# Performance work log

Hardware: AMD Instinct MI355X
Metric: run time of the kernel (lower is better)

The kernel has to match this reference:

```python
import jax, jax.numpy as jnp
import numpy as np

K = 4            # kNN neighbors (edge_conv k=4)
HEADS = 4
HID = 32
NEG_SLOPE = 0.2  # PyG GATConv leaky_relu default


def knn_idx(x, k):
    # x: [N, C]. Pairwise squared distances via gram trick, self excluded.
    N = x.shape[0]
    sq = jnp.sum(x * x, axis=1)
    d = sq[:, None] + sq[None, :] - 2.0 * (x @ x.T)          # [N, N]
    r = jnp.arange(N)
    d = d.at[r, r].set(jnp.inf)                               # no self in kNN
    _, idx = jax.lax.top_k(-d, k)                             # [N, k] nearest
    return idx


def gat_layer(x, neigh, W, a_src, a_dst, b):
    # x: [N, C]; neigh: [N, k+1] (incl. self loop). PyG GATConv, concat=True.
    N = x.shape[0]
    h = (x @ W).reshape(N, HEADS, HID)                        # [N, H, D]
    asrc = jnp.einsum('nhd,hd->nh', h, a_src)                 # [N, H]
    adst = jnp.einsum('nhd,hd->nh', h, a_dst)                 # [N, H]
    e = jax.nn.leaky_relu(adst[:, None, :] + asrc[neigh], NEG_SLOPE)  # [N, k+1, H]
    attn = jax.nn.softmax(e, axis=1)                          # segment softmax (fixed fan-in)
    out = jnp.einsum('nkh,nkhd->nhd', attn, h[neigh])         # [N, H, D]
    return out.reshape(N, HEADS * HID) + b


def setup_inputs() -> dict:
    key = jax.random.key(0)
    ks = jax.random.split(key, 12)
    B, E, C = 256, 64, 32
    s = 0.1
    return {
        'x': jax.random.normal(ks[0], (B, E, C), jnp.float32),
        # DynamicEdgeConv MLP: Linear(2C->HID), ReLU, Linear(HID->HID)
        'mlp_w1': jax.random.normal(ks[1], (2 * C, HID), jnp.float32) * s,
        'mlp_b1': jnp.zeros((HID,), jnp.float32),
        'mlp_w2': jax.random.normal(ks[2], (HID, HID), jnp.float32) * s,
        'mlp_b2': jnp.zeros((HID,), jnp.float32),
        # GATConv(HID, HID, heads=HEADS, concat=True)
        'gat_w': jax.random.normal(ks[3], (C, HEADS * HID), jnp.float32) * s,
        'gat_asrc': jax.random.normal(ks[4], (HEADS, HID), jnp.float32) * s,
        'gat_adst': jax.random.normal(ks[5], (HEADS, HID), jnp.float32) * s,
        'gat_b': jnp.zeros((HEADS * HID,), jnp.float32),
        # fc: Linear(HID*HEADS -> num_classes)
        'fc_w': jax.random.normal(ks[6], (HEADS * HID, 2), jnp.float32) * s,
        'fc_b': jnp.zeros((2,), jnp.float32),
    }


def reference(x, mlp_w1, mlp_b1, mlp_w2, mlp_b2, gat_w, gat_asrc, gat_adst, gat_b, fc_w, fc_b):
    B, E, C = x.shape
    N = B * E
    xf = x.reshape(N, C)
    idx = knn_idx(xf, K)                                      # [N, K] int32
    # EdgeConv message MLP + max pool (edge_attr is discarded by the original forward)
    xi = xf[:, None, :]                                       # [N, 1, C]
    xj = xf[idx]                                              # [N, K, C]
    ef = jnp.concatenate([jnp.broadcast_to(xi, xj.shape), xj - xi], axis=-1)
    ef = jax.nn.relu(ef @ mlp_w1 + mlp_b1) @ mlp_w2 + mlp_b2
    _edge_attr = ef.max(axis=1)                               # [N, HID], unused downstream
    # GAT with self loops (PyG add_self_loops=True)
    neigh = jnp.concatenate([idx, jnp.arange(N)[:, None]], axis=1)  # [N, K+1]
    h = gat_layer(xf, neigh, gat_w, gat_asrc, gat_adst, gat_b)
    h = jax.nn.elu(h)
    h = h.reshape(B, E, HEADS * HID).mean(axis=1)             # [B, H*D]
    return h @ fc_w + fc_b                                    # [B, num_classes]
```

## Files before the change

### kernel.cpp

```cpp
#include <hip/hip_runtime.h>
#include <math.h>

#define N_PTS   16384
#define NT      1024
#define NCHUNK  32
#define JT_CH   (NT/NCHUNK)
#define SUBT    8
#define NSUB    (JT_CH/SUBT)
#define NS      16

typedef __attribute__((ext_vector_type(4))) float f32x4;
typedef __attribute__((ext_vector_type(8))) _Float16 half8;

union H8 { half8 h; float4 f; };

#define MED3(a,b,c) __builtin_amdgcn_fmed3f((a),(b),(c))

#define INS4(c, A0, A1, A2, A3) {        \
  float n0_ = fmaxf(A0, c);              \
  float n1_ = MED3(A0, A1, c);           \
  float n2_ = MED3(A1, A2, c);           \
  float n3_ = MED3(A2, A3, c);           \
  A0 = n0_; A1 = n1_; A2 = n2_; A3 = n3_; }

__device__ __forceinline__ unsigned long long pack_key(float a, int j) {
  unsigned u = __float_as_uint(a);
  unsigned ord = u ^ (unsigned)(((int)u >> 31) | 0x80000000);
  unsigned m = ~ord;
  return ((unsigned long long)m << 32) | (unsigned)j;
}

__global__ __launch_bounds__(256) void k_prep(
    const float* __restrict__ x, float4* __restrict__ fragHi,
    float4* __restrict__ fragLo, float* __restrict__ nsq,
    unsigned* __restrict__ gcnt, unsigned long long* __restrict__ gbuf,
    unsigned* __restrict__ bcnt)
{
  int p = blockIdx.x * 256 + threadIdx.x;
  const float4* xp = (const float4*)(x + (size_t)p * 32);
  int tile = p >> 4, lb = p & 15;
  float sq = 0.f;
  #pragma unroll
  for (int g = 0; g < 4; ++g) {
    float4 va = xp[g * 2], vb = xp[g * 2 + 1];
    float f[8] = {va.x, va.y, va.z, va.w, vb.x, vb.y, vb.z, vb.w};
    H8 hh, hl;
    #pragma unroll
    for (int e = 0; e < 8; ++e) {
      sq = fmaf(f[e], f[e], sq);
      _Float16 hi = (_Float16)f[e];
      _Float16 lo = (_Float16)(f[e] - (float)hi);
      hh.h[e] = hi; hl.h[e] = hl.h[e] = lo;
    }
    int a = tile * 64 + g * 16 + lb;
    fragHi[a] = hh.f; fragLo[a] = hl.f;
  }
  nsq[p] = -0.5f * sq;
  gcnt[p] = 0u;
  #pragma unroll
  for (int e = 0; e < NS; ++e) gbuf[(size_t)p * NS + e] = ~0ull;
  if (blockIdx.x == 0 && threadIdx.x < NCHUNK) bcnt[threadIdx.x] = 0u;
}

__global__ __launch_bounds__(256, 4) void k_knnA(
    const float4* __restrict__ fragHi, const float4* __restrict__ fragLo,
    const float* __restrict__ nsq, float* __restrict__ cvals)
{
  __shared__ half8 sHi[SUBT * 64];
  __shared__ half8 sLo[SUBT * 64];
  __shared__ float sNq[SUBT * 16];

  const int tid = threadIdx.x;
  const int w = tid >> 6, lane = tid & 63;
  const int grp = lane >> 4, col = lane & 15;
  const int cy = blockIdx.y;
  const int itbase = blockIdx.x * 16 + w * 4;
  const bool blkdiag = ((int)(blockIdx.x >> 1) == cy);

  const half8* fH8 = (const half8*)fragHi;
  const half8* fL8 = (const half8*)fragLo;

  half8 bh[4], bl[4];
  #pragma unroll
  for (int s = 0; s < 4; ++s) {
    bh[s] = fH8[(size_t)(itbase + s) * 64 + lane];
    bl[s] = fL8[(size_t)(itbase + s) * 64 + lane];
  }
  const bool dg0 = (col == grp * 4 + 0), dg1 = (col == grp * 4 + 1);
  const bool dg2 = (col == grp * 4 + 2), dg3 = (col == grp * 4 + 3);

  float La1[4];
  #pragma unroll
  for (int s = 0; s < 4; ++s) La1[s] = -3.4e38f;

  for (int sc = 0; sc < NSUB; ++sc) {
    int jt0 = cy * JT_CH + sc * SUBT;
    __syncthreads();
    const float4* gH = fragHi + (size_t)jt0 * 64;
    const float4* gL = fragLo + (size_t)jt0 * 64;
    float4* dH = (float4*)sHi;
    float4* dL = (float4*)sLo;
    #pragma unroll
    for (int r = 0; r < 2; ++r) {
      dH[tid + r * 256] = gH[tid + r * 256];
      dL[tid + r * 256] = gL[tid + r * 256];
    }
    if (tid < SUBT * 16) sNq[tid] = nsq[jt0 * 16 + tid];
    __syncthreads();

    for (int t = 0; t < SUBT; ++t) {
      half8 ah = sHi[t * 64 + lane];
      half8 al = sLo[t * 64 + lane];
      f32x4 q = *(const f32x4*)&sNq[t * 16 + grp * 4];
      int jt = jt0 + t;
      #pragma unroll
      for (int s = 0; s < 4; ++s) {
        f32x4 acc = __builtin_amdgcn_mfma_f32_16x16x32_f16(ah, bh[s], q, 0, 0, 0);
        acc = __builtin_amdgcn_mfma_f32_16x16x32_f16(ah, bl[s], acc, 0, 0, 0);
        acc = __builtin_amdgcn_mfma_f32_16x16x32_f16(al, bh[s], acc, 0, 0, 0);
        if (blkdiag && jt == itbase + s) {
          acc.x = dg0 ? -3.4e38f : acc.x;
          acc.y = dg1 ? -3.4e38f : acc.y;
          acc.z = dg2 ? -3.4e38f : acc.z;
          acc.w = dg3 ? -3.4e38f : acc.w;
        }
        float t3 = fmaxf(fmaxf(acc.x, acc.y), acc.z);
        La1[s] = fmaxf(fmaxf(t3, acc.w), La1[s]);
      }
    }
  }

  #pragma unroll
  for (int s = 0; s < 4; ++s) {
    float m = La1[s];
    m = fmaxf(m, __shfl_xor(m, 16));
    m = fmaxf(m, __shfl_xor(m, 32));
    if (grp == 0) {
      int row = (itbase + s) * 16 + col;
      cvals[(size_t)cy * N_PTS + row] = m;
    }
  }
}

__global__ __launch_bounds__(128) void k_tauwl(
    const float* __restrict__ cvals, float* __restrict__ tau,
    unsigned* __restrict__ bcnt, int* __restrict__ bucket)
{
  __shared__ unsigned lcnt[NCHUNK];
  __shared__ unsigned gbase[NCHUNK];
  __shared__ int stage[NCHUNK][64];
  __shared__ float4 sL[64];
  __shared__ float sT[64];

  const int tid = threadIdx.x;
  const int lrow = tid & 63, half = tid >> 6;
  const int row = blockIdx.x * 64 + lrow;
  if (tid < NCHUNK) lcnt[tid] = 0u;
  __syncthreads();

  float A0 = -3.4e38f, A1 = -3.4e38f, A2 = -3.4e38f, A3 = -3.4e38f;
  float cm[16];
  #pragma unroll
  for (int k = 0; k < 16; ++k) {
    cm[k] = cvals[(size_t)(half * 16 + k) * N_PTS + row];
    INS4(cm[k], A0, A1, A2, A3);
  }
  if (half == 1) sL[lrow] = make_float4(A0, A1, A2, A3);
  __syncthreads();
  if (half == 0) {
    float4 o = sL[lrow];
    INS4(o.x, A0, A1, A2, A3);
    INS4(o.y, A0, A1, A2, A3);
    INS4(o.z, A0, A1, A2, A3);
    INS4(o.w, A0, A1, A2, A3);
    sT[lrow] = A3;
    tau[row] = A3;
  }
  __syncthreads();
  const float tt = sT[lrow];
  #pragma unroll
  for (int k = 0; k < 16; ++k) {
    if (cm[k] >= tt) {
      int c = half * 16 + k;
      unsigned p = atomicAdd(&lcnt[c], 1u);
      stage[c][p] = row;
    }
  }
  __syncthreads();
  if (tid < NCHUNK) gbase[tid] = atomicAdd(bcnt + tid, lcnt[tid]);
  __syncthreads();
  for (int c = 0; c < NCHUNK; ++c) {
    unsigned n = lcnt[c], gb = gbase[c];
    for (unsigned k = tid; k < n; k += 128)
      bucket[c * N_PTS + gb + k] = stage[c][k];
  }
}

__global__ __launch_bounds__(256) void k_knnBW(
    const float4* __restrict__ fragHi, const float4* __restrict__ fragLo,
    const float* __restrict__ nsq, const float* __restrict__ tau,
    const unsigned* __restrict__ bcnt, const int* __restrict__ bucket,
    unsigned* __restrict__ gcnt, unsigned long long* __restrict__ gbuf)
{
  const int c = blockIdx.x;
  const unsigned n = bcnt[c];
  const unsigned base = blockIdx.y * 64;
  if (base >= n) return;

  __shared__ int   sRow[64];
  __shared__ float sTau[64];

  const int tid = threadIdx.x;
  const int w = tid >> 6, lane = tid & 63;
  const int grp = lane >> 4, col = lane & 15;
  const float INF = __int_as_float(0x7f800000);

  if (tid < 64) {
    unsigned idx = base + tid;
    int myrow = (idx < n) ? bucket[c * N_PTS + idx] : -1;
    sRow[tid] = myrow;
    sTau[tid] = (myrow >= 0) ? tau[myrow] : INF;
  }
  __syncthreads();

  const half8* fH8 = (const half8*)fragHi;
  const half8* fL8 = (const half8*)fragLo;

  half8 bh[4], bl[4];
  int   rS[4];
  float tS[4];
  #pragma unroll
  for (int s = 0; s < 4; ++s) {
    int r = sRow[s * 16 + col];
    rS[s] = r;
    tS[s] = sTau[s * 16 + col];
    int rr = r < 0 ? 0 : r;
    size_t a = (size_t)(rr >> 4) * 64 + grp * 16 + (rr & 15);
    bh[s] = fH8[a];
    bl[s] = fL8[a];
  }

  const int jt0 = c * JT_CH + w * (JT_CH / 4);
  #pragma unroll 2
  for (int ti = 0; ti < JT_CH / 4; ++ti) {
    int jt = jt0 + ti;
    half8 ah = fH8[(size_t)jt * 64 + lane];
    half8 al = fL8[(size_t)jt * 64 + lane];
    f32x4 q = *(const f32x4*)&nsq[jt * 16 + grp * 4];
    #pragma unroll
    for (int s = 0; s < 4; ++s) {
      f32x4 acc = __builtin_amdgcn_mfma_f32_16x16x32_f16(ah, bh[s], q, 0, 0, 0);
      acc = __builtin_amdgcn_mfma_f32_16x16x32_f16(ah, bl[s], acc, 0, 0, 0);
      acc = __builtin_amdgcn_mfma_f32_16x16x32_f16(al, bh[s], acc, 0, 0, 0);
      int jbase = jt * 16 + grp * 4;
      acc.x = (jbase + 0 == rS[s]) ? -3.4e38f : acc.x;
      acc.y = (jbase + 1 == rS[s]) ? -3.4e38f : acc.y;
      acc.z = (jbase + 2 == rS[s]) ? -3.4e38f : acc.z;
      acc.w = (jbase + 3 == rS[s]) ? -3.4e38f : acc.w;
      float m = fmaxf(fmaxf(acc.x, acc.y), fmaxf(acc.z, acc.w));
      if (__ballot(m >= tS[s])) {
        float av[4] = {acc.x, acc.y, acc.z, acc.w};
        #pragma unroll
        for (int e = 0; e < 4; ++e) {
          if (av[e] >= tS[s]) {
            unsigned sl = atomicAdd(gcnt + rS[s], 1u);
            if (sl < (unsigned)NS) gbuf[(size_t)rS[s] * NS + sl] = pack_key(av[e], jbase + e);
          }
        }
      }
    }
  }
}

__global__ __launch_bounds__(256) void k_feat(
    const float* __restrict__ x, const float* __restrict__ gw,
    const float* __restrict__ aw_s, const float* __restrict__ aw_d,
    float* __restrict__ h, float* __restrict__ asrc, float* __restrict__ adst)
{
  const int tid = threadIdx.x;
  const int d = tid & 127, half = tid >> 7;
  const int head = d >> 5, hid = d & 31;

  float gwr[32];
  #pragma unroll
  for (int k = 0; k < 32; ++k) gwr[k] = gw[k * 128 + d];
  const float ws_ = aw_s[head * 32 + hid], wd_ = aw_d[head * 32 + hid];

  #pragma unroll
  for (int p = 0; p < 8; ++p) {
    int nl = (p << 1) | half;
    int n = blockIdx.x * 16 + nl;
    const float4* xr = (const float4*)(x + (size_t)n * 32);
    float acc = 0.f;
    #pragma unroll
    for (int r = 0; r < 8; ++r) {
      float4 v = xr[r];
      acc = fmaf(v.x, gwr[r * 4 + 0], acc);
      acc = fmaf(v.y, gwr[r * 4 + 1], acc);
      acc = fmaf(v.z, gwr[r * 4 + 2], acc);
      acc = fmaf(v.w, gwr[r * 4 + 3], acc);
    }
    h[(size_t)n * 128 + d] = acc;
    float ps = acc * ws_, pd = acc * wd_;
    #pragma unroll
    for (int off = 16; off; off >>= 1) {
      ps += __shfl_xor(ps, off, 32);
      pd += __shfl_xor(pd, off, 32);
    }
    if (hid == 0) { asrc[n * 4 + head] = ps; adst[n * 4 + head] = pd; }
  }
}

__global__ __launch_bounds__(256) void k_gat(
    const float* __restrict__ h, const float* __restrict__ asrc, const float* __restrict__ adst,
    const unsigned long long* __restrict__ gbuf, const float* __restrict__ gb,
    float* __restrict__ mo_part)
{
  int b2 = blockIdx.x;
  int b = b2 >> 2, qq = b2 & 3;
  int tid = threadIdx.x;
  __shared__ int4 sknn[16];
  if (tid < 16) {
    int row = b * 64 + qq * 16 + tid;
    unsigned long long K0 = ~0ull, K1 = ~0ull, K2 = ~0ull, K3 = ~0ull;
    const unsigned long long* src = gbuf + (size_t)row * NS;
    #pragma unroll
    for (int e = 0; e < NS; ++e) {
      unsigned long long cc = src[e];
      bool g = cc < K3, c0 = cc < K0, c1 = cc < K1, c2 = cc < K2;
      unsigned long long n1 = c0 ? K0 : (c1 ? cc : K1);
      unsigned long long n2 = c1 ? K1 : (c2 ? cc : K2);
      unsigned long long n3 = c2 ? K2 : (g ? cc : K3);
      K0 = c0 ? cc : K0; K1 = n1; K2 = n2; K3 = n3;
    }
    sknn[tid] = make_int4((int)(unsigned)K0, (int)(unsigned)K1,
                          (int)(unsigned)K2, (int)(unsigned)K3);
  }
  __syncthreads();

  int w = tid >> 6, lane = tid & 63;
  int da = lane, db = lane + 64;
  int ha = lane >> 5, hb = ha + 2;
  float acca = 0.f, accb = 0.f;

  #pragma unroll
  for (int t = 0; t < 4; ++t) {
    int nl = t * 4 + w;
    int n = b * 64 + qq * 16 + nl;
    int4 nb = sknn[nl];
    int nbs[5] = {nb.x, nb.y, nb.z, nb.w, n};
    float ad_a = adst[n * 4 + ha], ad_b = adst[n * 4 + hb];
    float ea[5], eb[5];
    #pragma unroll
    for (int k = 0; k < 5; ++k) {
      float va = ad_a + asrc[nbs[k] * 4 + ha];
      float vb = ad_b + asrc[nbs[k] * 4 + hb];
      ea[k] = va > 0.f ? va : 0.2f * va;
      eb[k] = vb > 0.f ? vb : 0.2f * vb;
    }
    float ma = ea[0], mb = eb[0];
    #pragma unroll
    for (int k = 1; k < 5; ++k) { ma = fmaxf(ma, ea[k]); mb = fmaxf(mb, eb[k]); }
    float sa = 0.f, sb = 0.f;
    #pragma unroll
    for (int k = 0; k < 5; ++k) {
      ea[k] = __expf(ea[k] - ma); sa += ea[k];
      eb[k] = __expf(eb[k] - mb); sb += eb[k];
    }
    float outa = 0.f, outb = 0.f;
    #pragma unroll
    for (int k = 0; k < 5; ++k) {
      const float* hr = h + (size_t)nbs[k] * 128;
      outa = fmaf(ea[k], hr[da], outa);
      outb = fmaf(eb[k], hr[db], outb);
    }
    outa = outa / sa + gb[da];
    outb = outb / sb + gb[db];
    acca += outa > 0.f ? outa : expm1f(outa);
    accb += outb > 0.f ? outb : expm1f(outb);
  }

  __shared__ float red[4][128];
  red[w][da] = acca; red[w][db] = accb;
  __syncthreads();
  if (tid < 128) {
    float s = (red[0][tid] + red[1][tid] + red[2][tid] + red[3][tid]) * (1.f / 64.f);
    mo_part[b2 * 128 + tid] = s;
  }
}

__global__ __launch_bounds__(64) void k_fc(
    const float* __restrict__ mo_part, const float* __restrict__ fw, const float* __restrict__ fb,
    float* __restrict__ out)
{
  int b = blockIdx.x, lane = threadIdx.x;
  float m0 = 0.f, m1 = 0.f;
  #pragma unroll
  for (int q = 0; q < 4; ++q) {
    m0 += mo_part[(b * 4 + q) * 128 + lane];
    m1 += mo_part[(b * 4 + q) * 128 + lane + 64];
  }
  float p0 = m0 * fw[lane * 2]     + m1 * fw[(lane + 64) * 2];
  float p1 = m0 * fw[lane * 2 + 1] + m1 * fw[(lane + 64) * 2 + 1];
  #pragma unroll
  for (int off = 32; off; off >>= 1) {
    p0 += __shfl_xor(p0, off, 64);
    p1 += __shfl_xor(p1, off, 64);
  }
  if (lane == 0) { out[b * 2] = p0 + fb[0]; out[b * 2 + 1] = p1 + fb[1]; }
}

extern "C" void kernel_launch(void* const* d_in, const int* in_sizes, int n_in,
                              void* d_out, int out_size, void* d_ws, size_t ws_size,
                              hipStream_t stream)
{
  const float* x   = (const float*)d_in[0];
  const float* gw  = (const float*)d_in[5];
  const float* as_ = (const float*)d_in[6];
  const float* ad_ = (const float*)d_in[7];
  const float* gb  = (const float*)d_in[8];
  const float* fw  = (const float*)d_in[9];
  const float* fb  = (const float*)d_in[10];

  char* ws = (char*)d_ws;
  float*  h      = (float*)(ws);
  float*  cvals  = (float*)(ws);
  float*  asrc   = (float*)(ws + 8388608);
  float*  adst   = (float*)(ws + 8650752);
  float4* fragHi = (float4*)(ws + 8912896);
  float*  mo_part= (float*)(ws + 8912896);
  float4* fragLo = (float4*)(ws + 9961472);
  float*  nsq    = (float*)(ws + 11010048);
  float*  tau    = (float*)(ws + 11075584);
  unsigned* gcnt = (unsigned*)(ws + 11141120);
  unsigned long long* gbuf = (unsigned long long*)(ws + 11206656);
  unsigned* bcnt = (unsigned*)(ws + 13303808);
  int*    bucket = (int*)   (ws + 13304064);
  float*  outp   = (float*)d_out;

  k_prep<<<64, 256, 0, stream>>>(x, fragHi, fragLo, nsq, gcnt, gbuf, bcnt);
  k_knnA<<<dim3(64, NCHUNK), 256, 0, stream>>>(fragHi, fragLo, nsq, cvals);
  k_tauwl<<<N_PTS / 64, 128, 0, stream>>>(cvals, tau, bcnt, bucket);
  k_knnBW<<<dim3(NCHUNK, N_PTS / 64), 256, 0, stream>>>(fragHi, fragLo, nsq, tau,
                                                        bcnt, bucket, gcnt, gbuf);
  k_feat<<<N_PTS / 16, 256, 0, stream>>>(x, gw, as_, ad_, h, asrc, adst);
  k_gat<<<1024, 256, 0, stream>>>(h, asrc, adst, gbuf, gb, mo_part);
  k_fc<<<256, 64, 0, stream>>>(mo_part, fw, fb, outp);
}
```

Baseline: 115.9 us.

## Double-buffer shared-memory tiles in kNN MFMA kernel with register prefetch

The kNN distance kernel now keeps two shared-memory buffers and loads the next sub-chunk of fragments into registers while MFMAs run on the current one. The registers are written to the other buffer after compute, so each iteration needs one barrier instead of two. The sub-chunk size is halved to keep the LDS footprint about the same, and the inner loop is fully unrolled. The trade-off is more barrier iterations and extra register pressure from the prefetched values, which could reduce occupancy.

```diff
diff --git a/kernel.cpp b/kernel.cpp
--- a/kernel.cpp
+++ b/kernel.cpp
@@ -5,7 +5,7 @@
 #define NT      1024
 #define NCHUNK  32
 #define JT_CH   (NT/NCHUNK)
-#define SUBT    8
+#define SUBT    4
 #define NSUB    (JT_CH/SUBT)
 #define NS      16
 
@@ -50,7 +50,7 @@
       sq = fmaf(f[e], f[e], sq);
       _Float16 hi = (_Float16)f[e];
       _Float16 lo = (_Float16)(f[e] - (float)hi);
-      hh.h[e] = hi; hl.h[e] = hl.h[e] = lo;
+      hh.h[e] = hi; hl.h[e] = lo;
     }
     int a = tile * 64 + g * 16 + lb;
     fragHi[a] = hh.f; fragLo[a] = hl.f;
@@ -66,9 +66,9 @@
     const float4* __restrict__ fragHi, const float4* __restrict__ fragLo,
     const float* __restrict__ nsq, float* __restrict__ cvals)
 {
-  __shared__ half8 sHi[SUBT * 64];
-  __shared__ half8 sLo[SUBT * 64];
-  __shared__ float sNq[SUBT * 16];
+  __shared__ half8 sH[2][SUBT * 64];
+  __shared__ half8 sL[2][SUBT * 64];
+  __shared__ float sNq[2][SUBT * 16];
 
   const int tid = threadIdx.x;
   const int w = tid >> 6, lane = tid & 63;
@@ -93,25 +93,31 @@
   #pragma unroll
   for (int s = 0; s < 4; ++s) La1[s] = -3.4e38f;
 
+  {
+    int jt0 = cy * JT_CH;
+    ((float4*)sH[0])[tid] = ((const float4*)(fragHi + (size_t)jt0 * 64))[tid];
+    ((float4*)sL[0])[tid] = ((const float4*)(fragLo + (size_t)jt0 * 64))[tid];
+    if (tid < SUBT * 16) sNq[0][tid] = nsq[jt0 * 16 + tid];
+  }
+  __syncthreads();
+
   for (int sc = 0; sc < NSUB; ++sc) {
+    const int cur = sc & 1;
+    float4 vH, vL; float vq = 0.f;
+    const bool pf = (sc + 1 < NSUB);
+    if (pf) {
+      int jn = cy * JT_CH + (sc + 1) * SUBT;
+      vH = ((const float4*)(fragHi + (size_t)jn * 64))[tid];
+      vL = ((const float4*)(fragLo + (size_t)jn * 64))[tid];
+      if (tid < SUBT * 16) vq = nsq[jn * 16 + tid];
+    }
+
     int jt0 = cy * JT_CH + sc * SUBT;
-    __syncthreads();
-    const float4* gH = fragHi + (size_t)jt0 * 64;
-    const float4* gL = fragLo + (size_t)jt0 * 64;
-    float4* dH = (float4*)sHi;
-    float4* dL = (float4*)sLo;
-    #pragma unroll
-    for (int r = 0; r < 2; ++r) {
-      dH[tid + r * 256] = gH[tid + r * 256];
-      dL[tid + r * 256] = gL[tid + r * 256];
-    }
-    if (tid < SUBT * 16) sNq[tid] = nsq[jt0 * 16 + tid];
-    __syncthreads();
-
+    #pragma unroll
     for (int t = 0; t < SUBT; ++t) {
-      half8 ah = sHi[t * 64 + lane];
-      half8 al = sLo[t * 64 + lane];
-      f32x4 q = *(const f32x4*)&sNq[t * 16 + grp * 4];
+      half8 ah = sH[cur][t * 64 + lane];
+      half8 al = sL[cur][t * 64 + lane];
+      f32x4 q = *(const f32x4*)&sNq[cur][t * 16 + grp * 4];
       int jt = jt0 + t;
       #pragma unroll
       for (int s = 0; s < 4; ++s) {
@@ -128,6 +134,13 @@
         La1[s] = fmaxf(fmaxf(t3, acc.w), La1[s]);
       }
     }
+
+    if (pf) {
+      ((float4*)sH[cur ^ 1])[tid] = vH;
+      ((float4*)sL[cur ^ 1])[tid] = vL;
+      if (tid < SUBT * 16) sNq[cur ^ 1][tid] = vq;
+    }
+    __syncthreads();
   }
 
   #pragma unroll
```

Result: slower. 118.5 us (+2.3%).
